# Optimization experiments

Measured on AMD Instinct MI355X. Metric: run time of the kernel, lower is better.

## Reference

```python
import jax, jax.numpy as jnp
import numpy as np

# dims matching init_kwargs
B, C, T = 64, 8, 2048
K, DIL = 16, 4            # kernel_size, dilation
MLP = 16                  # mlp_dim
NF = min(MLP, K // 2 + 1) # n_frequencies = 9
FEAT = C * NF * 2         # 144
H1, H2 = 64, 32           # ReLUBlock hidden dims (64 -> 64//2)
EFF = DIL * (K - 1)       # 60
W = T - EFF               # 1988 windows


def setup_inputs() -> dict:
    key = jax.random.key(0)
    ks = jax.random.split(key, 10)
    def lin(k, out_d, in_d):
        kw, kb = jax.random.split(k)
        bound = 1.0 / np.sqrt(in_d)
        w = jax.random.uniform(kw, (out_d, in_d), jnp.float32, -bound, bound)
        b = jax.random.uniform(kb, (out_d,), jnp.float32, -bound, bound)
        return w, b
    x = jax.random.normal(ks[0], (B, C, T), jnp.float32)
    proj_w, proj_b = lin(ks[1], MLP, FEAT)
    w1, b1 = lin(ks[2], H1, MLP)
    w2, b2 = lin(ks[3], H2, H1)
    out_w, out_b = lin(ks[4], 1, H2)
    agg_w = jax.random.normal(ks[5], (W,), jnp.float32) * 0.1
    return {"x": x, "proj_w": proj_w, "proj_b": proj_b, "w1": w1, "b1": b1,
            "w2": w2, "b2": b2, "out_w": out_w, "out_b": out_b, "agg_w": agg_w}


def reference(x, proj_w, proj_b, w1, b1, w2, b2, out_w, out_b, agg_w):
    # Build all dilated windows at once: window[t, j] = x[..., t - (K-1-j)*DIL]
    starts = jnp.arange(EFF, T)                      # [W]
    offs = -(K - 1 - jnp.arange(K)) * DIL            # [K]
    idx = starts[:, None] + offs[None, :]            # [W, K]
    win = x[:, :, idx]                               # [B, C, W, K]
    f = jnp.fft.rfft(win, axis=-1)[..., :NF]         # [B, C, W, NF]
    mag = jnp.log1p(jnp.abs(f))
    ph = jnp.angle(f) / jnp.pi
    feat = jnp.stack([mag, ph], axis=-1)             # [B, C, W, NF, 2]
    feat = feat.transpose(0, 2, 1, 3, 4).reshape(B, W, FEAT)  # [B, W, C*NF*2]
    p = jnp.tanh(feat @ proj_w.T + proj_b) * jnp.pi  # [B, W, MLP]
    h = jax.nn.relu(p @ w1.T + b1)                   # [B, W, H1]
    h = jax.nn.relu(h @ w2.T + b2)                   # [B, W, H2]
    out = (h @ out_w.T + out_b)[..., 0]              # [B, W]
    wts = jax.nn.softmax(agg_w)                      # [W]
    return (out * wts[None, :]).sum(axis=1)          # [B]
```

## Files before the change

kernel.cpp:

```cpp
#include <hip/hip_runtime.h>
#include <math.h>

#define B_    64
#define C_    8
#define T_    2048
#define K_    16
#define NF_   9
#define FEAT_ 144
#define MLP_  16
#define H1_   64
#define H2_   32
#define EFF_  60
#define W_    1988
#define NWCH_ 8
#define PI_F  3.14159265358979323846f

constexpr float COS16[16] = {
   1.0f,  0.92387953251128674f,  0.70710678118654752f,  0.38268343236508977f,
   0.0f, -0.38268343236508977f, -0.70710678118654752f, -0.92387953251128674f,
  -1.0f, -0.92387953251128674f, -0.70710678118654752f, -0.38268343236508977f,
   0.0f,  0.38268343236508977f,  0.70710678118654752f,  0.92387953251128674f };
constexpr float SIN16[16] = {
   0.0f,  0.38268343236508977f,  0.70710678118654752f,  0.92387953251128674f,
   1.0f,  0.92387953251128674f,  0.70710678118654752f,  0.38268343236508977f,
   0.0f, -0.38268343236508977f, -0.70710678118654752f, -0.92387953251128674f,
   0.0f, -0.92387953251128674f, -0.70710678118654752f, -0.38268343236508977f };
constexpr float SIN16F[16] = {
   0.0f,  0.38268343236508977f,  0.70710678118654752f,  0.92387953251128674f,
   1.0f,  0.92387953251128674f,  0.70710678118654752f,  0.38268343236508977f,
   0.0f, -0.38268343236508977f, -0.70710678118654752f, -0.92387953251128674f,
  -1.0f, -0.92387953251128674f, -0.70710678118654752f, -0.38268343236508977f };

__device__ __forceinline__ float fast_log1p(float s) {
  return __builtin_amdgcn_logf(1.0f + s) * 0.69314718055994531f;
}

__device__ __forceinline__ float atanpi_poly(float r) {
  const float s2 = r * r;
  float p = -0.0037310f;
  p = fmaf(p, s2,  0.0167600f);
  p = fmaf(p, s2, -0.0370617f);
  p = fmaf(p, s2,  0.0616068f);
  p = fmaf(p, s2, -0.10587734f);
  p = fmaf(p, s2,  0.31830265f);
  return r * p;
}

__device__ __forceinline__ float atan2pi_fast(float im, float re) {
  const float ax = fabsf(re), ay = fabsf(im);
  const float mx = fmaxf(ax, ay), mn = fminf(ax, ay);
  const float r = mn * __builtin_amdgcn_rcpf(fmaxf(mx, 1e-37f));
  float t = atanpi_poly(r);
  t = (ay > ax) ? 0.5f - t : t;
  t = (__float_as_uint(re) & 0x80000000u) ? 1.0f - t : t;
  return copysignf(t, im);
}

__device__ __forceinline__ float fast_tanh(float z) {
  const float az = fabsf(z);
  const float e = __builtin_amdgcn_exp2f(-2.8853900817779268f * az);
  const float th = fmaf(-2.0f, e * __builtin_amdgcn_rcpf(1.0f + e), 1.0f);
  return copysignf(th, z);
}

__global__ __launch_bounds__(256) void prep_kernel(const float* __restrict__ pw,
                                                   const float* __restrict__ w2,
                                                   float* __restrict__ PWt,
                                                   float* __restrict__ W2t) {
  const int tid = blockIdx.x * 256 + threadIdx.x;
  if (tid < MLP_ * FEAT_) {
    const int j = tid / FEAT_, f = tid - j * FEAT_;
    PWt[f * MLP_ + j] = pw[tid];
  }
  if (tid < H2_ * H1_) {
    const int m = tid >> 6, i = tid & 63;
    W2t[i * H2_ + m] = w2[tid];
  }
}

__global__ __launch_bounds__(256) void softmax_kernel(const float* __restrict__ agg,
                                                      float* __restrict__ wts) {
  __shared__ float red[256];
  const int tid = threadIdx.x;
  float m = -INFINITY;
  for (int i = tid; i < W_; i += 256) m = fmaxf(m, agg[i]);
  red[tid] = m; __syncthreads();
  for (int s = 128; s > 0; s >>= 1) { if (tid < s) red[tid] = fmaxf(red[tid], red[tid+s]); __syncthreads(); }
  const float mx = red[0];
  __syncthreads();
  float sum = 0.f;
  for (int i = tid; i < W_; i += 256) sum += expf(agg[i] - mx);
  red[tid] = sum; __syncthreads();
  for (int s = 128; s > 0; s >>= 1) { if (tid < s) red[tid] += red[tid+s]; __syncthreads(); }
  const float inv = 1.f / red[0];
  for (int i = tid; i < W_; i += 256) wts[i] = expf(agg[i] - mx) * inv;
}

__global__ __launch_bounds__(256) void tcn_main(
    const float* __restrict__ x,
    const float* __restrict__ PWt, const float* __restrict__ proj_b,
    const float* __restrict__ w1, const float* __restrict__ b1,
    const float* __restrict__ W2t, const float* __restrict__ b2,
    const float* __restrict__ out_w, const float* __restrict__ out_b,
    const float* __restrict__ wts, float* __restrict__ partials) {
  __shared__ float red[256];
  const int tid = threadIdx.x;
  const int b = blockIdx.y;
  const int w = blockIdx.x * 256 + tid;
  float val = 0.f;
  if (w < W_) {
    float pacc[MLP_];
    #pragma unroll
    for (int j = 0; j < MLP_; j++) pacc[j] = proj_b[j];

    const float* xb = x + (size_t)(b * C_) * T_ + w;
    #pragma unroll 1
    for (int c = 0; c < C_; c++) {
      const float* xc = xb + c * T_;
      float win[K_];
      #pragma unroll
      for (int k = 0; k < K_; k++) win[k] = xc[k * 4];

      float ae[8], bo[8];
      #pragma unroll
      for (int k = 0; k < 8; k++) { ae[k] = win[k] + win[k+8]; bo[k] = win[k] - win[k+8]; }

      #pragma unroll
      for (int n = 0; n < NF_; n++) {
        float re = 0.f, im = 0.f;
        #pragma unroll
        for (int k = 0; k < 8; k++) {
          const float v = (n & 1) ? bo[k] : ae[k];
          const int t = (n * k) & 15;
          re = fmaf(v,  COS16[t],  re);
          im = fmaf(v, -SIN16F[t], im);
        }
        const float m2  = fmaf(re, re, im * im);
        const float s   = __builtin_amdgcn_sqrtf(m2);
        const float mag = fast_log1p(s);
        const float ph  = atan2pi_fast(im, re);

        const float* rm = PWt + (size_t)((c * NF_ + n) * 2) * MLP_;
        #pragma unroll
        for (int j = 0; j < MLP_; j++)
          pacc[j] = fmaf(mag, rm[j], fmaf(ph, rm[MLP_ + j], pacc[j]));
      }
    }

    float p[MLP_];
    #pragma unroll
    for (int j = 0; j < MLP_; j++) p[j] = fast_tanh(pacc[j]) * PI_F;

    float h2a[H2_];
    #pragma unroll
    for (int m = 0; m < H2_; m++) h2a[m] = b2[m];

    #pragma unroll 8
    for (int i = 0; i < H1_; i++) {
      const float* r1 = w1 + i * MLP_;
      float acc = b1[i];
      #pragma unroll
      for (int j = 0; j < MLP_; j++) acc = fmaf(p[j], r1[j], acc);
      const float h1v = fmaxf(acc, 0.f);
      const float* r2 = W2t + i * H2_;
      #pragma unroll
      for (int m = 0; m < H2_; m++) h2a[m] = fmaf(h1v, r2[m], h2a[m]);
    }

    float o = out_b[0];
    #pragma unroll
    for (int m = 0; m < H2_; m++) o = fmaf(fmaxf(h2a[m], 0.f), out_w[m], o);
    val = o * wts[w];
  }

  red[tid] = val; __syncthreads();
  for (int s = 128; s > 0; s >>= 1) { if (tid < s) red[tid] += red[tid+s]; __syncthreads(); }
  if (tid == 0) partials[b * gridDim.x + blockIdx.x] = red[0];
}

__global__ void finalize_kernel(const float* __restrict__ partials, float* __restrict__ out) {
  const int b = threadIdx.x;
  if (b < B_) {
    float s = 0.f;
    #pragma unroll
    for (int c = 0; c < NWCH_; c++) s += partials[b * NWCH_ + c];
    out[b] = s;
  }
}

extern "C" void kernel_launch(void* const* d_in, const int* in_sizes, int n_in,
                              void* d_out, int out_size, void* d_ws, size_t ws_size,
                              hipStream_t stream) {
  const float* x      = (const float*)d_in[0];
  const float* proj_w = (const float*)d_in[1];
  const float* proj_b = (const float*)d_in[2];
  const float* w1     = (const float*)d_in[3];
  const float* b1     = (const float*)d_in[4];
  const float* w2     = (const float*)d_in[5];
  const float* b2     = (const float*)d_in[6];
  const float* out_w  = (const float*)d_in[7];
  const float* out_b  = (const float*)d_in[8];
  const float* agg_w  = (const float*)d_in[9];

  float* wts      = (float*)d_ws;
  float* partials = (float*)d_ws + 2048;
  float* PWt      = (float*)d_ws + 4096;
  float* W2t      = (float*)d_ws + 4096 + 2304;

  prep_kernel<<<9, 256, 0, stream>>>(proj_w, w2, PWt, W2t);
  softmax_kernel<<<1, 256, 0, stream>>>(agg_w, wts);
  tcn_main<<<dim3(NWCH_, B_), 256, 0, stream>>>(x, PWt, proj_b, w1, b1, W2t, b2,
                                                out_w, out_b, wts, partials);
  finalize_kernel<<<1, 64, 0, stream>>>(partials, (float*)d_out);
}
```

Measured before the change: 60.71 us.

## Merge setup kernels, stage MLP weights in LDS, and process channel pairs

Merges the softmax and weight-transpose kernels into one setup launch, which removes a kernel launch. In the main kernel, w1, W2t and b1 are staged in shared memory and read as float4 in the MLP loop, where they were previously read from global/scalar memory. The DFT loop now handles two channels per iteration to raise instruction-level parallelism. The costs are higher register pressure, an extra barrier, and LDS fill work in every block.

```diff
diff --git a/kernel.cpp b/kernel.cpp
--- a/kernel.cpp
+++ b/kernel.cpp
@@ -20,11 +20,6 @@
    0.0f, -0.38268343236508977f, -0.70710678118654752f, -0.92387953251128674f,
   -1.0f, -0.92387953251128674f, -0.70710678118654752f, -0.38268343236508977f,
    0.0f,  0.38268343236508977f,  0.70710678118654752f,  0.92387953251128674f };
-constexpr float SIN16[16] = {
-   0.0f,  0.38268343236508977f,  0.70710678118654752f,  0.92387953251128674f,
-   1.0f,  0.92387953251128674f,  0.70710678118654752f,  0.38268343236508977f,
-   0.0f, -0.38268343236508977f, -0.70710678118654752f, -0.92387953251128674f,
-   0.0f, -0.92387953251128674f, -0.70710678118654752f, -0.38268343236508977f };
 constexpr float SIN16F[16] = {
    0.0f,  0.38268343236508977f,  0.70710678118654752f,  0.92387953251128674f,
    1.0f,  0.92387953251128674f,  0.70710678118654752f,  0.38268343236508977f,
@@ -63,37 +58,38 @@
   return copysignf(th, z);
 }
 
-__global__ __launch_bounds__(256) void prep_kernel(const float* __restrict__ pw,
-                                                   const float* __restrict__ w2,
-                                                   float* __restrict__ PWt,
-                                                   float* __restrict__ W2t) {
-  const int tid = blockIdx.x * 256 + threadIdx.x;
-  if (tid < MLP_ * FEAT_) {
-    const int j = tid / FEAT_, f = tid - j * FEAT_;
-    PWt[f * MLP_ + j] = pw[tid];
+__global__ __launch_bounds__(256) void setup_kernel(const float* __restrict__ agg,
+                                                    float* __restrict__ wts,
+                                                    const float* __restrict__ pw,
+                                                    const float* __restrict__ w2,
+                                                    float* __restrict__ PWt,
+                                                    float* __restrict__ W2t) {
+  if (blockIdx.x == 0) {
+    __shared__ float red[256];
+    const int tid = threadIdx.x;
+    float m = -INFINITY;
+    for (int i = tid; i < W_; i += 256) m = fmaxf(m, agg[i]);
+    red[tid] = m; __syncthreads();
+    for (int s = 128; s > 0; s >>= 1) { if (tid < s) red[tid] = fmaxf(red[tid], red[tid+s]); __syncthreads(); }
+    const float mx = red[0];
+    __syncthreads();
+    float sum = 0.f;
+    for (int i = tid; i < W_; i += 256) sum += expf(agg[i] - mx);
+    red[tid] = sum; __syncthreads();
+    for (int s = 128; s > 0; s >>= 1) { if (tid < s) red[tid] += red[tid+s]; __syncthreads(); }
+    const float inv = 1.f / red[0];
+    for (int i = tid; i < W_; i += 256) wts[i] = expf(agg[i] - mx) * inv;
+  } else {
+    const int tid = (blockIdx.x - 1) * 256 + threadIdx.x;
+    if (tid < MLP_ * FEAT_) {
+      const int j = tid / FEAT_, f = tid - j * FEAT_;
+      PWt[f * MLP_ + j] = pw[tid];
+    }
+    if (tid < H2_ * H1_) {
+      const int m = tid >> 6, i = tid & 63;
+      W2t[i * H2_ + m] = w2[tid];
+    }
   }
-  if (tid < H2_ * H1_) {
-    const int m = tid >> 6, i = tid & 63;
-    W2t[i * H2_ + m] = w2[tid];
-  }
-}
-
-__global__ __launch_bounds__(256) void softmax_kernel(const float* __restrict__ agg,
-                                                      float* __restrict__ wts) {
-  __shared__ float red[256];
-  const int tid = threadIdx.x;
-  float m = -INFINITY;
-  for (int i = tid; i < W_; i += 256) m = fmaxf(m, agg[i]);
-  red[tid] = m; __syncthreads();
-  for (int s = 128; s > 0; s >>= 1) { if (tid < s) red[tid] = fmaxf(red[tid], red[tid+s]); __syncthreads(); }
-  const float mx = red[0];
-  __syncthreads();
-  float sum = 0.f;
-  for (int i = tid; i < W_; i += 256) sum += expf(agg[i] - mx);
-  red[tid] = sum; __syncthreads();
-  for (int s = 128; s > 0; s >>= 1) { if (tid < s) red[tid] += red[tid+s]; __syncthreads(); }
-  const float inv = 1.f / red[0];
-  for (int i = tid; i < W_; i += 256) wts[i] = expf(agg[i] - mx) * inv;
 }
 
 __global__ __launch_bounds__(256) void tcn_main(
@@ -103,8 +99,17 @@
     const float* __restrict__ W2t, const float* __restrict__ b2,
     const float* __restrict__ out_w, const float* __restrict__ out_b,
     const float* __restrict__ wts, float* __restrict__ partials) {
+  __shared__ __align__(16) float W1s[H1_ * MLP_];
+  __shared__ __align__(16) float W2s[H1_ * H2_];
+  __shared__ float B1s[H1_];
   __shared__ float red[256];
+
   const int tid = threadIdx.x;
+  for (int idx = tid; idx < H1_ * MLP_; idx += 256) W1s[idx] = w1[idx];
+  for (int idx = tid; idx < H1_ * H2_; idx += 256) W2s[idx] = W2t[idx];
+  if (tid < H1_) B1s[tid] = b1[tid];
+  __syncthreads();
+
   const int b = blockIdx.y;
   const int w = blockIdx.x * 256 + tid;
   float val = 0.f;
@@ -115,35 +120,48 @@
 
     const float* xb = x + (size_t)(b * C_) * T_ + w;
     #pragma unroll 1
-    for (int c = 0; c < C_; c++) {
-      const float* xc = xb + c * T_;
-      float win[K_];
-      #pragma unroll
-      for (int k = 0; k < K_; k++) win[k] = xc[k * 4];
-
-      float ae[8], bo[8];
-      #pragma unroll
-      for (int k = 0; k < 8; k++) { ae[k] = win[k] + win[k+8]; bo[k] = win[k] - win[k+8]; }
+    for (int cp = 0; cp < 4; cp++) {
+      const float* xc0 = xb + (2 * cp) * T_;
+      const float* xc1 = xb + (2 * cp + 1) * T_;
+      float win0[K_], win1[K_];
+      #pragma unroll
+      for (int k = 0; k < K_; k++) win0[k] = xc0[k * 4];
+      #pragma unroll
+      for (int k = 0; k < K_; k++) win1[k] = xc1[k * 4];
+
+      float ae0[8], bo0[8], ae1[8], bo1[8];
+      #pragma unroll
+      for (int k = 0; k < 8; k++) {
+        ae0[k] = win0[k] + win0[k+8]; bo0[k] = win0[k] - win0[k+8];
+        ae1[k] = win1[k] + win1[k+8]; bo1[k] = win1[k] - win1[k+8];
+      }
 
       #pragma unroll
       for (int n = 0; n < NF_; n++) {
-        float re = 0.f, im = 0.f;
+        float re0 = 0.f, im0 = 0.f, re1 = 0.f, im1 = 0.f;
         #pragma unroll
         for (int k = 0; k < 8; k++) {
-          const float v = (n & 1) ? bo[k] : ae[k];
           const int t = (n * k) & 15;
-          re = fmaf(v,  COS16[t],  re);
-          im = fmaf(v, -SIN16F[t], im);
+          const float cv = COS16[t], sv = -SIN16F[t];
+          const float v0 = (n & 1) ? bo0[k] : ae0[k];
+          const float v1 = (n & 1) ? bo1[k] : ae1[k];
+          re0 = fmaf(v0, cv, re0); im0 = fmaf(v0, sv, im0);
+          re1 = fmaf(v1, cv, re1); im1 = fmaf(v1, sv, im1);
         }
-        const float m2  = fmaf(re, re, im * im);
-        const float s   = __builtin_amdgcn_sqrtf(m2);
-        const float mag = fast_log1p(s);
-        const float ph  = atan2pi_fast(im, re);
-
-        const float* rm = PWt + (size_t)((c * NF_ + n) * 2) * MLP_;
+        const float s0   = __builtin_amdgcn_sqrtf(fmaf(re0, re0, im0 * im0));
+        const float s1   = __builtin_amdgcn_sqrtf(fmaf(re1, re1, im1 * im1));
+        const float mag0 = fast_log1p(s0);
+        const float mag1 = fast_log1p(s1);
+        const float ph0  = atan2pi_fast(im0, re0);
+        const float ph1  = atan2pi_fast(im1, re1);
+
+        const float* rm0 = PWt + (size_t)(((2*cp)   * NF_ + n) * 2) * MLP_;
+        const float* rm1 = PWt + (size_t)(((2*cp+1) * NF_ + n) * 2) * MLP_;
         #pragma unroll
-        for (int j = 0; j < MLP_; j++)
-          pacc[j] = fmaf(mag, rm[j], fmaf(ph, rm[MLP_ + j], pacc[j]));
+        for (int j = 0; j < MLP_; j++) {
+          pacc[j] = fmaf(mag0, rm0[j], fmaf(ph0, rm0[MLP_ + j], pacc[j]));
+          pacc[j] = fmaf(mag1, rm1[j], fmaf(ph1, rm1[MLP_ + j], pacc[j]));
+        }
       }
     }
 
@@ -155,16 +173,28 @@
     #pragma unroll
     for (int m = 0; m < H2_; m++) h2a[m] = b2[m];
 
-    #pragma unroll 8
+    #pragma unroll 4
     for (int i = 0; i < H1_; i++) {
-      const float* r1 = w1 + i * MLP_;
-      float acc = b1[i];
-      #pragma unroll
-      for (int j = 0; j < MLP_; j++) acc = fmaf(p[j], r1[j], acc);
+      const float4* r1 = reinterpret_cast<const float4*>(&W1s[i * MLP_]);
+      float acc = B1s[i];
+      #pragma unroll
+      for (int q = 0; q < 4; q++) {
+        const float4 a = r1[q];
+        acc = fmaf(p[4*q+0], a.x, acc);
+        acc = fmaf(p[4*q+1], a.y, acc);
+        acc = fmaf(p[4*q+2], a.z, acc);
+        acc = fmaf(p[4*q+3], a.w, acc);
+      }
       const float h1v = fmaxf(acc, 0.f);
-      const float* r2 = W2t + i * H2_;
-      #pragma unroll
-      for (int m = 0; m < H2_; m++) h2a[m] = fmaf(h1v, r2[m], h2a[m]);
+      const float4* r2 = reinterpret_cast<const float4*>(&W2s[i * H2_]);
+      #pragma unroll
+      for (int q = 0; q < 8; q++) {
+        const float4 a = r2[q];
+        h2a[4*q+0] = fmaf(h1v, a.x, h2a[4*q+0]);
+        h2a[4*q+1] = fmaf(h1v, a.y, h2a[4*q+1]);
+        h2a[4*q+2] = fmaf(h1v, a.z, h2a[4*q+2]);
+        h2a[4*q+3] = fmaf(h1v, a.w, h2a[4*q+3]);
+      }
     }
 
     float o = out_b[0];
@@ -175,7 +205,7 @@
 
   red[tid] = val; __syncthreads();
   for (int s = 128; s > 0; s >>= 1) { if (tid < s) red[tid] += red[tid+s]; __syncthreads(); }
-  if (tid == 0) partials[b * gridDim.x + blockIdx.x] = red[0];
+  if (tid == 0) partials[b * NWCH_ + blockIdx.x] = red[0];
 }
 
 __global__ void finalize_kernel(const float* __restrict__ partials, float* __restrict__ out) {
@@ -207,8 +237,7 @@
   float* PWt      = (float*)d_ws + 4096;
   float* W2t      = (float*)d_ws + 4096 + 2304;
 
-  prep_kernel<<<9, 256, 0, stream>>>(proj_w, w2, PWt, W2t);
-  softmax_kernel<<<1, 256, 0, stream>>>(agg_w, wts);
+  setup_kernel<<<10, 256, 0, stream>>>(agg_w, wts, proj_w, w2, PWt, W2t);
   tcn_main<<<dim3(NWCH_, B_), 256, 0, stream>>>(x, PWt, proj_b, w1, b1, W2t, b2,
                                                 out_w, out_b, wts, partials);
   finalize_kernel<<<1, 64, 0, stream>>>(partials, (float*)d_out);
```

Result: slower. 68.53 us (+12.9%).
